# Performance work log

Measured on AMD Instinct MI355X. Metric: run time of the kernel, lower is better.

Reference implementation:

```python
import jax, jax.numpy as jnp
import numpy as np

WIN = 7
NP_ = WIN * WIN
COV_NORM = NP_ / (NP_ - 1)

def _box(x, w):
    # valid 7x7 box filter, NCHW, single channel
    return jax.lax.conv_general_dilated(
        x, w, window_strides=(1, 1), padding='VALID',
        dimension_numbers=('NCHW', 'OIHW', 'NCHW'))

def setup_inputs() -> dict:
    key = jax.random.key(0)
    k1, k2, k3, k4 = jax.random.split(key, 4)
    N, H, W = 64, 384, 384
    X = jax.random.uniform(k1, (N, 1, H, W), dtype=jnp.float32)
    Y = jax.random.uniform(k2, (N, 1, H, W), dtype=jnp.float32)
    norm = jax.random.uniform(k3, (N,), dtype=jnp.float32)
    mx = jax.random.uniform(k4, (N,), dtype=jnp.float32) + 0.5
    w = jnp.ones((1, 1, WIN, WIN), dtype=jnp.float32) / NP_
    return {"X": X, "Y": Y, "norm": norm, "max": mx, "w": w}

def reference(X, Y, norm, max, w):
    q = 100000.0
    X = X * q
    Y = Y * q
    mx = max * q
    data_range = mx[:, None, None, None]
    C1 = (0.01 * data_range) ** 2
    C2 = (0.03 * data_range) ** 2
    ux = _box(X, w)
    uy = _box(Y, w)
    uxx = _box(X * X, w)
    uyy = _box(Y * Y, w)
    uxy = _box(X * Y, w)
    vx = COV_NORM * (uxx - ux * ux)
    vy = COV_NORM * (uyy - uy * uy)
    vxy = COV_NORM * (uxy - ux * uy)
    A1 = 2 * ux * uy + C1
    A2 = 2 * vxy + C2
    B1 = ux ** 2 + uy ** 2 + C1
    B2 = vx + vy + C2
    S = (A1 * A2) / (B1 * B2)
    return -jnp.mean(S)
```

## Files before the change

kernel.cpp:

```cpp
#include <hip/hip_runtime.h>


constexpr int IND   = 384;
constexpr int OUTD  = 378;
constexpr int RB    = 14;
constexpr int BANDS = OUTD / RB;
constexpr int CPL   = 6;

using f32x2 = __attribute__((ext_vector_type(2))) float;

__global__ __launch_bounds__(64, 2)
void ssim_band(const float* __restrict__ X, const float* __restrict__ Y,
               const float* __restrict__ MX, float* __restrict__ blocksum)
{
    const int band = blockIdx.x;
    const int n    = blockIdx.y;
    const int lane = threadIdx.x;
    const int c0   = lane * CPL;
    const int r0   = band * RB;

    const float* __restrict__ Xp = X + (size_t)n * (IND * IND) + c0;
    const float* __restrict__ Yp = Y + (size_t)n * (IND * IND) + c0;

    float hx[7][CPL], hy[7][CPL];
    float sx[CPL]  = {}, sy[CPL]  = {};
    float sxx[CPL] = {}, syy[CPL] = {}, sxy[CPL] = {};

#define LOADROW(DX, DY, R) {                                                  \
    const float* _px = Xp + (size_t)(R) * IND;                                \
    const float* _py = Yp + (size_t)(R) * IND;                                \
    f32x2 _a = *(const f32x2*)_px;                                            \
    f32x2 _b = *(const f32x2*)(_px + 2);                                      \
    f32x2 _c = *(const f32x2*)(_px + 4);                                      \
    f32x2 _d = *(const f32x2*)_py;                                            \
    f32x2 _e = *(const f32x2*)(_py + 2);                                      \
    f32x2 _f = *(const f32x2*)(_py + 4);                                      \
    DX[0]=_a.x; DX[1]=_a.y; DX[2]=_b.x; DX[3]=_b.y; DX[4]=_c.x; DX[5]=_c.y;   \
    DY[0]=_d.x; DY[1]=_d.y; DY[2]=_e.x; DY[3]=_e.y; DY[4]=_f.x; DY[5]=_f.y; }

#pragma unroll
    for (int k = 0; k < 6; ++k) LOADROW(hx[k], hy[k], r0 + k)

    float pax[CPL], pay[CPL], pbx[CPL], pby[CPL];
    LOADROW(pax, pay, r0 + 6)
    LOADROW(pbx, pby, r0 + 7)

#pragma unroll
    for (int k = 0; k < 6; ++k)
#pragma unroll
        for (int c = 0; c < CPL; ++c) {
            float x = hx[k][c], y = hy[k][c];
            sx[c] += x;  sy[c] += y;
            sxx[c] = fmaf(x, x, sxx[c]);
            syy[c] = fmaf(y, y, syy[c]);
            sxy[c] = fmaf(x, y, sxy[c]);
        }

    const float m   = MX[n];
    const float c1  = (0.01f * m) * (0.01f * m);
    const float c2  = (0.03f * m) * (0.03f * m);
    const float k1  = 2401.0f * c1;
    const float k2  = 2401.0f * c2;
    const float cn  = 49.0f / 48.0f;
    const float cn2 = 2.0f * cn;

#define PHASE_A(S, NP, CS) {                                                  \
    float _p1 = S[0];                                                         \
    float _p2 = _p1 + S[1];                                                   \
    float _p3 = _p2 + S[2];                                                   \
    float _p4 = _p3 + S[3];                                                   \
    float _p5 = _p4 + S[4];                                                   \
    float _p6 = _p5 + S[5];                                                   \
    NP[0] = __shfl_down(_p1, 1);                                              \
    NP[1] = __shfl_down(_p2, 1);                                              \
    NP[2] = __shfl_down(_p3, 1);                                              \
    NP[3] = __shfl_down(_p4, 1);                                              \
    NP[4] = __shfl_down(_p5, 1);                                              \
    NP[5] = __shfl_down(_p6, 1);                                              \
    CS[5] = S[5];                                                             \
    CS[4] = S[4] + S[5];                                                      \
    CS[3] = S[3] + CS[4];                                                     \
    CS[2] = S[2] + CS[3];                                                     \
    CS[1] = S[1] + CS[2];                                                     \
    CS[0] = _p6; }

    float partial = 0.f;

#pragma unroll 1
    for (int kk = 0; kk < RB / 7; ++kk) {
#pragma unroll
        for (int i = 0; i < 7; ++i) {
            const int os = i;
            const int ws = (i + 6) % 7;

#pragma unroll
            for (int c = 0; c < CPL; ++c) {
                float nx = pax[c], ny = pay[c];
                sx[c] += nx;  sy[c] += ny;
                sxx[c] = fmaf(nx, nx, sxx[c]);
                syy[c] = fmaf(ny, ny, syy[c]);
                sxy[c] = fmaf(nx, ny, sxy[c]);
            }
            float u[CPL];
#pragma unroll
            for (int c = 0; c < CPL; ++c) u[c] = sxx[c] + syy[c];

            float np1[CPL], np2[CPL], np5[CPL], np34[CPL];
            float cs1[CPL], cs2[CPL], cs5[CPL], cs34[CPL];
            PHASE_A(sx,  np1,  cs1)
            PHASE_A(sy,  np2,  cs2)
            PHASE_A(sxy, np5,  cs5)
            PHASE_A(u,   np34, cs34)

#pragma unroll
            for (int c = 0; c < CPL; ++c) {
                float ox = hx[os][c], oy = hy[os][c];
                float nx = pax[c],    ny = pay[c];
                sx[c] -= ox;  sy[c] -= oy;
                sxx[c] = fmaf(-ox, ox, sxx[c]);
                syy[c] = fmaf(-oy, oy, syy[c]);
                sxy[c] = fmaf(-ox, oy, sxy[c]);
                hx[ws][c] = nx;  hy[ws][c] = ny;
                pax[c] = pbx[c]; pay[c] = pby[c];
            }
            {
                int nr = r0 + 7 * kk + i + 8;
                if (nr > IND - 1) nr = IND - 1;
                LOADROW(pbx, pby, nr)
            }

            if (lane < 63) {
#pragma unroll
                for (int c = 0; c < CPL; ++c) {
                    float t1  = cs1[c]  + np1[c];
                    float t2  = cs2[c]  + np2[c];
                    float t5  = cs5[c]  + np5[c];
                    float t34 = cs34[c] + np34[c];
                    float pxy = t1 * t2;
                    float ss  = fmaf(t1, t1, t2 * t2);
                    float A1  = fmaf(2.f, pxy, k1);
                    float B1  = ss + k1;
                    float A2  = fmaf(cn2, fmaf(49.f, t5, -pxy), k2);
                    float B2  = fmaf(cn, fmaf(49.f, t34, -ss), k2);
                    partial += __fdividef(A1 * A2, B1 * B2);
                }
            }
        }
    }
#undef PHASE_A
#undef LOADROW

#pragma unroll
    for (int off = 32; off; off >>= 1) partial += __shfl_down(partial, off);
    if (lane == 0) blocksum[(size_t)n * BANDS + band] = partial;
}

__global__ __launch_bounds__(256)
void ssim_reduce(const float* __restrict__ blocksum, float* __restrict__ out,
                 int nblocks, float inv_npix)
{
    const int tid = threadIdx.x;
    float s = 0.f;
    for (int i = tid; i < nblocks; i += 256) s += blocksum[i];
#pragma unroll
    for (int off = 32; off; off >>= 1) s += __shfl_down(s, off);
    __shared__ float ws[4];
    if ((tid & 63) == 0) ws[tid >> 6] = s;
    __syncthreads();
    if (tid == 0) out[0] = -(ws[0] + ws[1] + ws[2] + ws[3]) * inv_npix;
}

extern "C" void kernel_launch(void* const* d_in, const int* in_sizes, int n_in,
                              void* d_out, int out_size, void* d_ws, size_t ws_size,
                              hipStream_t stream)
{
    const float* X  = (const float*)d_in[0];
    const float* Y  = (const float*)d_in[1];
    const float* MX = (const float*)d_in[3];

    const int N       = in_sizes[3];
    const int nblocks = N * BANDS;

    float* bs = (float*)d_ws;

    dim3 grid(BANDS, N);
    ssim_band<<<grid, 64, 0, stream>>>(X, Y, MX, bs);

    const float inv_npix = 1.0f / ((float)N * OUTD * OUTD);
    ssim_reduce<<<1, 256, 0, stream>>>(bs, (float*)d_out, nblocks, inv_npix);
}
```

Baseline: 29.13 us.

## Split band into two interleaved 7-row streams and reload departing rows instead of keeping history

Each 14-row band is now processed as two independent sliding-window streams of 7 output rows, interleaved per iteration. Only a two-deep prefetch queue of outgoing and incoming rows is kept, and outgoing rows are re-read from global memory or cache, so the 7-row history array is gone. The aim is more instruction-level parallelism from two independent dependency chains and fewer registers spent on history, which could help occupancy. In exchange each input row is loaded twice, adding memory traffic, and the two streams bring extra accumulator and prefetch state.

```diff
diff --git a/kernel.cpp b/kernel.cpp
--- a/kernel.cpp
+++ b/kernel.cpp
@@ -22,47 +22,37 @@
     const float* __restrict__ Xp = X + (size_t)n * (IND * IND) + c0;
     const float* __restrict__ Yp = Y + (size_t)n * (IND * IND) + c0;
 
-    float hx[7][CPL], hy[7][CPL];
-    float sx[CPL]  = {}, sy[CPL]  = {};
-    float sxx[CPL] = {}, syy[CPL] = {}, sxy[CPL] = {};
-
 #define LOADROW(DX, DY, R) {                                                  \
     const float* _px = Xp + (size_t)(R) * IND;                                \
     const float* _py = Yp + (size_t)(R) * IND;                                \
-    f32x2 _a = *(const f32x2*)_px;                                            \
-    f32x2 _b = *(const f32x2*)(_px + 2);                                      \
+    f32x2 _a = *(const f32x2*)_px;   f32x2 _b = *(const f32x2*)(_px + 2);     \
     f32x2 _c = *(const f32x2*)(_px + 4);                                      \
-    f32x2 _d = *(const f32x2*)_py;                                            \
-    f32x2 _e = *(const f32x2*)(_py + 2);                                      \
+    f32x2 _d = *(const f32x2*)_py;   f32x2 _e = *(const f32x2*)(_py + 2);     \
     f32x2 _f = *(const f32x2*)(_py + 4);                                      \
     DX[0]=_a.x; DX[1]=_a.y; DX[2]=_b.x; DX[3]=_b.y; DX[4]=_c.x; DX[5]=_c.y;   \
     DY[0]=_d.x; DY[1]=_d.y; DY[2]=_e.x; DY[3]=_e.y; DY[4]=_f.x; DY[5]=_f.y; }
 
-#pragma unroll
-    for (int k = 0; k < 6; ++k) LOADROW(hx[k], hy[k], r0 + k)
-
-    float pax[CPL], pay[CPL], pbx[CPL], pby[CPL];
-    LOADROW(pax, pay, r0 + 6)
-    LOADROW(pbx, pby, r0 + 7)
-
-#pragma unroll
-    for (int k = 0; k < 6; ++k)
-#pragma unroll
-        for (int c = 0; c < CPL; ++c) {
-            float x = hx[k][c], y = hy[k][c];
-            sx[c] += x;  sy[c] += y;
-            sxx[c] = fmaf(x, x, sxx[c]);
-            syy[c] = fmaf(y, y, syy[c]);
-            sxy[c] = fmaf(x, y, sxy[c]);
-        }
-
-    const float m   = MX[n];
-    const float c1  = (0.01f * m) * (0.01f * m);
-    const float c2  = (0.03f * m) * (0.03f * m);
-    const float k1  = 2401.0f * c1;
-    const float k2  = 2401.0f * c2;
-    const float cn  = 49.0f / 48.0f;
-    const float cn2 = 2.0f * cn;
+#define ACCROW(SX,SY,SXX,SYY,SXY, RX,RY)                                      \
+    _Pragma("unroll")                                                         \
+    for (int c = 0; c < CPL; ++c) {                                           \
+        float x = RX[c], y = RY[c];                                           \
+        SX[c] += x;  SY[c] += y;                                              \
+        SXX[c] = fmaf(x, x, SXX[c]);                                          \
+        SYY[c] = fmaf(y, y, SYY[c]);                                          \
+        SXY[c] = fmaf(x, y, SXY[c]); }
+
+#define SUBROW(SX,SY,SXX,SYY,SXY, RX,RY)                                      \
+    _Pragma("unroll")                                                         \
+    for (int c = 0; c < CPL; ++c) {                                           \
+        float x = RX[c], y = RY[c];                                           \
+        SX[c] -= x;  SY[c] -= y;                                              \
+        SXX[c] = fmaf(-x, x, SXX[c]);                                         \
+        SYY[c] = fmaf(-y, y, SYY[c]);                                         \
+        SXY[c] = fmaf(-x, y, SXY[c]); }
+
+#define COPYROW(DX,DY, SX,SY)                                                 \
+    _Pragma("unroll")                                                         \
+    for (int c = 0; c < CPL; ++c) { DX[c] = SX[c]; DY[c] = SY[c]; }
 
 #define PHASE_A(S, NP, CS) {                                                  \
     float _p1 = S[0];                                                         \
@@ -84,70 +74,97 @@
     CS[1] = S[1] + CS[2];                                                     \
     CS[0] = _p6; }
 
+    float sxA[CPL]={}, syA[CPL]={}, sxxA[CPL]={}, syyA[CPL]={}, sxyA[CPL]={};
+    float naxA[CPL], nayA[CPL], nbxA[CPL], nbyA[CPL];
+    float oaxA[CPL], oayA[CPL], obxA[CPL], obyA[CPL];
+    float sxB[CPL]={}, syB[CPL]={}, sxxB[CPL]={}, syyB[CPL]={}, sxyB[CPL]={};
+    float naxB[CPL], nayB[CPL], nbxB[CPL], nbyB[CPL];
+    float oaxB[CPL], oayB[CPL], obxB[CPL], obyB[CPL];
+
+    LOADROW(oaxA, oayA, r0 + 0)
+    LOADROW(obxA, obyA, r0 + 1)
+    LOADROW(naxA, nayA, r0 + 6)
+    LOADROW(nbxA, nbyA, r0 + 7)
+    LOADROW(oaxB, oayB, r0 + 7)
+    LOADROW(obxB, obyB, r0 + 8)
+    LOADROW(naxB, nayB, r0 + 13)
+    LOADROW(nbxB, nbyB, r0 + 14)
+
+    ACCROW(sxA,syA,sxxA,syyA,sxyA, oaxA,oayA)
+    ACCROW(sxA,syA,sxxA,syyA,sxyA, obxA,obyA)
+#pragma unroll
+    for (int k = 2; k < 6; ++k) {
+        float tx[CPL], ty[CPL];
+        LOADROW(tx, ty, r0 + k)
+        ACCROW(sxA,syA,sxxA,syyA,sxyA, tx,ty)
+    }
+    ACCROW(sxB,syB,sxxB,syyB,sxyB, oaxB,oayB)
+    ACCROW(sxB,syB,sxxB,syyB,sxyB, obxB,obyB)
+#pragma unroll
+    for (int k = 9; k < 13; ++k) {
+        float tx[CPL], ty[CPL];
+        LOADROW(tx, ty, r0 + k)
+        ACCROW(sxB,syB,sxxB,syyB,sxyB, tx,ty)
+    }
+
+    const float m   = MX[n];
+    const float c1  = (0.01f * m) * (0.01f * m);
+    const float c2  = (0.03f * m) * (0.03f * m);
+    const float k1  = 2401.0f * c1;
+    const float k2  = 2401.0f * c2;
+    const float cn  = 49.0f / 48.0f;
+    const float cn2 = 2.0f * cn;
+
     float partial = 0.f;
 
+#define STREAMSTEP(sx,sy,sxx,syy,sxy, nax,nay,nbx,nby, oax,oay,obx,oby, OLDR, NEWR) \
+    {                                                                         \
+        ACCROW(sx,sy,sxx,syy,sxy, nax,nay)                                    \
+        float u[CPL];                                                         \
+        _Pragma("unroll")                                                     \
+        for (int c = 0; c < CPL; ++c) u[c] = sxx[c] + syy[c];                 \
+        float np1[CPL], np2[CPL], np5[CPL], np34[CPL];                        \
+        float cs1[CPL], cs2[CPL], cs5[CPL], cs34[CPL];                        \
+        PHASE_A(sx,  np1,  cs1)                                               \
+        PHASE_A(sy,  np2,  cs2)                                               \
+        PHASE_A(sxy, np5,  cs5)                                               \
+        PHASE_A(u,   np34, cs34)                                              \
+        SUBROW(sx,sy,sxx,syy,sxy, oax,oay)                                    \
+        COPYROW(oax,oay, obx,oby)                                             \
+        COPYROW(nax,nay, nbx,nby)                                             \
+        { int _r = (OLDR); LOADROW(obx,oby, _r) }                             \
+        { int _r = (NEWR); if (_r > IND - 1) _r = IND - 1;                    \
+          LOADROW(nbx,nby, _r) }                                              \
+        if (lane < 63) {                                                      \
+            _Pragma("unroll")                                                 \
+            for (int c = 0; c < CPL; ++c) {                                   \
+                float t1  = cs1[c]  + np1[c];                                 \
+                float t2  = cs2[c]  + np2[c];                                 \
+                float t5  = cs5[c]  + np5[c];                                 \
+                float t34 = cs34[c] + np34[c];                                \
+                float pxy = t1 * t2;                                          \
+                float ss  = fmaf(t1, t1, t2 * t2);                            \
+                float A1  = fmaf(2.f, pxy, k1);                               \
+                float B1  = ss + k1;                                          \
+                float A2  = fmaf(cn2, fmaf(49.f, t5, -pxy), k2);              \
+                float B2  = fmaf(cn,  fmaf(49.f, t34, -ss), k2);              \
+                partial += __fdividef(A1 * A2, B1 * B2);                      \
+            }                                                                 \
+        }                                                                     \
+    }
+
 #pragma unroll 1
-    for (int kk = 0; kk < RB / 7; ++kk) {
-#pragma unroll
-        for (int i = 0; i < 7; ++i) {
-            const int os = i;
-            const int ws = (i + 6) % 7;
-
-#pragma unroll
-            for (int c = 0; c < CPL; ++c) {
-                float nx = pax[c], ny = pay[c];
-                sx[c] += nx;  sy[c] += ny;
-                sxx[c] = fmaf(nx, nx, sxx[c]);
-                syy[c] = fmaf(ny, ny, syy[c]);
-                sxy[c] = fmaf(nx, ny, sxy[c]);
-            }
-            float u[CPL];
-#pragma unroll
-            for (int c = 0; c < CPL; ++c) u[c] = sxx[c] + syy[c];
-
-            float np1[CPL], np2[CPL], np5[CPL], np34[CPL];
-            float cs1[CPL], cs2[CPL], cs5[CPL], cs34[CPL];
-            PHASE_A(sx,  np1,  cs1)
-            PHASE_A(sy,  np2,  cs2)
-            PHASE_A(sxy, np5,  cs5)
-            PHASE_A(u,   np34, cs34)
-
-#pragma unroll
-            for (int c = 0; c < CPL; ++c) {
-                float ox = hx[os][c], oy = hy[os][c];
-                float nx = pax[c],    ny = pay[c];
-                sx[c] -= ox;  sy[c] -= oy;
-                sxx[c] = fmaf(-ox, ox, sxx[c]);
-                syy[c] = fmaf(-oy, oy, syy[c]);
-                sxy[c] = fmaf(-ox, oy, sxy[c]);
-                hx[ws][c] = nx;  hy[ws][c] = ny;
-                pax[c] = pbx[c]; pay[c] = pby[c];
-            }
-            {
-                int nr = r0 + 7 * kk + i + 8;
-                if (nr > IND - 1) nr = IND - 1;
-                LOADROW(pbx, pby, nr)
-            }
-
-            if (lane < 63) {
-#pragma unroll
-                for (int c = 0; c < CPL; ++c) {
-                    float t1  = cs1[c]  + np1[c];
-                    float t2  = cs2[c]  + np2[c];
-                    float t5  = cs5[c]  + np5[c];
-                    float t34 = cs34[c] + np34[c];
-                    float pxy = t1 * t2;
-                    float ss  = fmaf(t1, t1, t2 * t2);
-                    float A1  = fmaf(2.f, pxy, k1);
-                    float B1  = ss + k1;
-                    float A2  = fmaf(cn2, fmaf(49.f, t5, -pxy), k2);
-                    float B2  = fmaf(cn, fmaf(49.f, t34, -ss), k2);
-                    partial += __fdividef(A1 * A2, B1 * B2);
-                }
-            }
-        }
-    }
+    for (int i = 0; i < 7; ++i) {
+        STREAMSTEP(sxA,syA,sxxA,syyA,sxyA, naxA,nayA,nbxA,nbyA,
+                   oaxA,oayA,obxA,obyA, r0 + i + 2, r0 + i + 8)
+        STREAMSTEP(sxB,syB,sxxB,syyB,sxyB, naxB,nayB,nbxB,nbyB,
+                   oaxB,oayB,obxB,obyB, r0 + i + 9, r0 + i + 15)
+    }
+#undef STREAMSTEP
 #undef PHASE_A
+#undef COPYROW
+#undef SUBROW
+#undef ACCROW
 #undef LOADROW
 
 #pragma unroll
```

New measurement: 42.36 us. +45.4%, slower.
